# Optimization experiments

Measured on AMD Instinct MI355X. Metric: run time of the kernel, lower is better.

## Reference

```python
import jax, jax.numpy as jnp
import numpy as np

EPS = 1e-5  # torch LayerNorm default


def _ln(x, g, b):
    m = x.mean(-1, keepdims=True)
    v = ((x - m) ** 2).mean(-1, keepdims=True)
    return (x - m) / jnp.sqrt(v + EPS) * g + b


def setup_inputs() -> dict:
    B, T, D, H, L = 4, 2048, 512, 8, 2
    key = jax.random.key(0)
    ks = jax.random.split(key, 16)
    w = lambda k, shp, fan: jax.random.normal(k, shp, jnp.float32) * (fan ** -0.5)
    return {
        "x_vid": jax.random.normal(ks[0], (B, T, D), jnp.float32),
        "x_aud": jax.random.normal(ks[1], (B, T, D), jnp.float32),
        "vid_kpm": jax.random.bernoulli(ks[2], 0.1, (B, T)),
        "aud_kpm": jax.random.bernoulli(ks[3], 0.1, (B, T)),
        "Wq_vid": w(ks[4], (L, D, D), D),
        "Wk_aud_for_vid": w(ks[5], (L, D, D), D),
        "Wq_aud": w(ks[6], (L, D, D), D),
        "Wk_vid_for_aud": w(ks[7], (L, D, D), D),
        "vg_W1": w(ks[8], (L, 2 * H, H), H),
        "vg_b1": jnp.zeros((L, 2 * H), jnp.float32),
        "vg_W2": w(ks[9], (L, 1, 2 * H), 2 * H),
        "vg_b2": jnp.zeros((L, 1), jnp.float32),
        "ag_W1": w(ks[10], (L, 2 * H, H), H),
        "ag_b1": jnp.zeros((L, 2 * H), jnp.float32),
        "ag_W2": w(ks[11], (L, 1, 2 * H), 2 * H),
        "ag_b2": jnp.zeros((L, 1), jnp.float32),
        "vid_ln_g": jnp.ones((L, D), jnp.float32),
        "vid_ln_b": jnp.zeros((L, D), jnp.float32),
        "aud_ln_g": jnp.ones((L, D), jnp.float32),
        "aud_ln_b": jnp.zeros((L, D), jnp.float32),
    }


def reference(x_vid, x_aud, vid_kpm, aud_kpm,
              Wq_vid, Wk_aud_for_vid, Wq_aud, Wk_vid_for_aud,
              vg_W1, vg_b1, vg_W2, vg_b2,
              ag_W1, ag_b1, ag_W2, ag_b2,
              vid_ln_g, vid_ln_b, aud_ln_g, aud_ln_b):
    B, T, D = x_vid.shape
    L = Wq_vid.shape[0]
    H = vg_W1.shape[-1]
    dh = D // H
    scale = dh ** -0.5

    def heads(x):  # (B,T,D) -> (B,H,T,dh)
        return x.reshape(B, T, H, dh).transpose(0, 2, 1, 3)

    # mask-derived constants
    aud_valid = jnp.clip((~aud_kpm).sum(-1).astype(jnp.float32), 1.0)[:, None, None]  # (B,1,1)
    vid_valid = jnp.clip((~vid_kpm).sum(-1).astype(jnp.float32), 1.0)[:, None, None]
    aud_all = aud_kpm.all(-1)  # (B,)
    vid_all = vid_kpm.all(-1)

    def gate_mlp(rel, W1, b1, W2, b2):  # rel: (B,T,H) -> (B,T,1)
        h1 = jax.nn.relu(jnp.einsum('bth,eh->bte', rel, W1) + b1)
        return jax.nn.sigmoid(jnp.einsum('bte,oe->bto', h1, W2) + b2)

    for i in range(L):
        # --- vid gated by attention to aud (NOTE: source applies vid_norms to BOTH) ---
        vid_n = _ln(x_vid, vid_ln_g[i], vid_ln_b[i])
        aud_n = _ln(x_aud, vid_ln_g[i], vid_ln_b[i])
        q = heads(jnp.einsum('btd,od->bto', vid_n, Wq_vid[i]))
        k = heads(jnp.einsum('btd,od->bto', aud_n, Wk_aud_for_vid[i]))
        logits = jnp.einsum('bhtd,bhsd->bhts', q, k) * scale  # (B,H,T,T)
        logits = jnp.where(aud_kpm[:, None, None, :], 0.0, logits)
        rel = logits.sum(-1) / aud_valid           # (B,H,T)
        rel = rel.transpose(0, 2, 1)               # (B,T,H)
        gate_v = gate_mlp(rel, vg_W1[i], vg_b1[i], vg_W2[i], vg_b2[i])
        gate_v = jnp.where(aud_all[:, None, None], 0.0, gate_v)
        x_vid = x_vid + x_vid * gate_v             # dropout is identity at eval

        # --- aud gated by attention to (updated) vid; source applies aud_norms to BOTH ---
        aud_n = _ln(x_aud, aud_ln_g[i], aud_ln_b[i])
        vid_n = _ln(x_vid, aud_ln_g[i], aud_ln_b[i])
        q = heads(jnp.einsum('btd,od->bto', aud_n, Wq_aud[i]))
        k = heads(jnp.einsum('btd,od->bto', vid_n, Wk_vid_for_aud[i]))
        logits = jnp.einsum('bhtd,bhsd->bhts', q, k) * scale
        logits = jnp.where(vid_kpm[:, None, None, :], 0.0, logits)
        rel = (logits.sum(-1) / vid_valid).transpose(0, 2, 1)
        gate_a = gate_mlp(rel, ag_W1[i], ag_b1[i], ag_W2[i], ag_b2[i])
        gate_a = jnp.where(vid_all[:, None, None], 0.0, gate_a)
        x_aud = x_aud + x_aud * gate_a

    return (x_vid, x_aud)
```

## Files before the change

### kernel.cpp

```cpp
#include <hip/hip_runtime.h>
#include <math.h>

#define BB 4
#define TT 2048
#define DD 512
#define HH 8
#define EPS 1e-5f
#define SCALE 0.125f
#define WW ((size_t)DD * DD)


__device__ __forceinline__ float wred(float s) {
#pragma unroll
  for (int o = 32; o > 0; o >>= 1) s += __shfl_xor(s, o);
  return s;
}

__device__ __forceinline__ void ldf(const float* p, int lane, float f[8]) {
  float4 a = *reinterpret_cast<const float4*>(p + lane * 4);
  float4 c = *reinterpret_cast<const float4*>(p + 256 + lane * 4);
  f[0]=a.x; f[1]=a.y; f[2]=a.z; f[3]=a.w;
  f[4]=c.x; f[5]=c.y; f[6]=c.z; f[7]=c.w;
}

__global__ __launch_bounds__(256) void sums_kernel(
    const float* __restrict__ xv, const float* __restrict__ xa,
    const int* __restrict__ vkpm, const int* __restrict__ akpm,
    float* __restrict__ partial)
{
  const int blk  = blockIdx.x;
  const int s    = blk >> 8;
  const int b    = (blk >> 6) & 3;
  const int tile = blk & 63;
  const int wave = threadIdx.x >> 6, lane = threadIdx.x & 63;
  const float* x  = s ? xa : xv;
  const int* kpm  = s ? akpm : vkpm;
  const int row0  = b * TT + tile * 32 + wave * 8;

  __shared__ float lds[4][DD];

  float acc[8] = {0.f,0.f,0.f,0.f,0.f,0.f,0.f,0.f};
  for (int r = 0; r < 8; ++r) {
    const int row = row0 + r;
    float v[8]; ldf(x + (size_t)row * DD, lane, v);
    float s1 = 0.f, s2 = 0.f;
#pragma unroll
    for (int k = 0; k < 8; ++k) { s1 += v[k]; s2 += v[k]*v[k]; }
    s1 = wred(s1); s2 = wred(s2);
    const float mean = s1 * (1.f / (float)DD);
    const float var  = s2 * (1.f / (float)DD) - mean * mean;
    const float rstd = rsqrtf(var + EPS);
    if (kpm[row] == 0) {
#pragma unroll
      for (int k = 0; k < 8; ++k) acc[k] += (v[k] - mean) * rstd;
    }
  }
#pragma unroll
  for (int k = 0; k < 4; ++k) {
    lds[wave][lane*4+k]       = acc[k];
    lds[wave][256+lane*4+k]   = acc[4+k];
  }
  __syncthreads();
  const int tid = threadIdx.x;
  float s0 = lds[0][tid] + lds[1][tid] + lds[2][tid] + lds[3][tid];
  float s1 = lds[0][tid+256] + lds[1][tid+256] + lds[2][tid+256] + lds[3][tid+256];
  float* p = partial + ((size_t)(s*4 + b) * 64 + tile) * DD;
  p[tid]       = s0;
  p[tid + 256] = s1;
}

__global__ __launch_bounds__(256) void reduce_kernel(
    const float* __restrict__ partial,
    const int* __restrict__ vkpm, const int* __restrict__ akpm,
    float* __restrict__ S, float* __restrict__ fs)
{
  const int tid = threadIdx.x, wave = tid >> 6, lane = tid & 63;
  const int job = blockIdx.x * 4 + wave;
  const int sb  = job >> 7;
  const int d0  = (job & 127) * 4;
  __shared__ float csh[4];

  const float* p0 = partial + ((size_t)sb * 64 + lane) * DD + d0;
  float4 a = *reinterpret_cast<const float4*>(p0);
  a.x = wred(a.x); a.y = wred(a.y); a.z = wred(a.z); a.w = wred(a.w);
  if (lane == 0) *reinterpret_cast<float4*>(S + (size_t)sb * DD + d0) = a;

  if (blockIdx.x < 8) {
    const int s = blockIdx.x >> 2, b = blockIdx.x & 3;
    const int* mk = s ? akpm : vkpm;
    int cnt = 0;
#pragma unroll
    for (int q = 0; q < 8; ++q) cnt += (mk[b*TT + q*256 + tid] == 0) ? 1 : 0;
    float fc = wred((float)cnt);
    if (lane == 0) csh[wave] = fc;
    __syncthreads();
    if (tid == 0) {
      const float vc = csh[0] + csh[1] + csh[2] + csh[3];
      fs[blockIdx.x*4 + 0] = SCALE / fmaxf(vc, 1.f);
      fs[blockIdx.x*4 + 1] = (vc > 0.f) ? 1.f : 0.f;
      fs[blockIdx.x*4 + 2] = vc;
    }
  }
}

__global__ __launch_bounds__(256) void mphase_kernel(
    const float* __restrict__ S, const float* __restrict__ fs,
    const float* __restrict__ Wq_v, const float* __restrict__ Wk_av,
    const float* __restrict__ Wq_a, const float* __restrict__ Wk_va,
    const float* __restrict__ vid_g, const float* __restrict__ vid_b,
    const float* __restrict__ aud_g, const float* __restrict__ aud_b,
    float* __restrict__ mp,
    float* __restrict__ cv,
    float* __restrict__ smv)
{
  const int blk = blockIdx.x;
  const int p = blk >> 5, b = (blk >> 3) & 3, h = blk & 7;
  const int layer = p >> 1;
  const int isA = ((p & 1) == 0);
  const int tid = threadIdx.x, wave = tid >> 6, lane = tid & 63;
  __shared__ float ksl[64];
  __shared__ float cs2[4], ss2[4];

  const int ksb = (isA ? 1 : 0) * 4 + b;
  const float* g  = (isA ? vid_g : aud_g) + (size_t)layer * DD;
  const float* be = (isA ? vid_b : aud_b) + (size_t)layer * DD;
  const float* Wk = (isA ? Wk_av : Wk_va) + (size_t)layer * WW;
  const float* Wq = (isA ? Wq_v  : Wq_a ) + (size_t)layer * WW;
  const float fac  = fs[ksb*4 + 0];
  const float cntf = fs[ksb*4 + 2];

  float gv[8], bv[8], sv[8], nl[8];
  ldf(g, lane, gv); ldf(be, lane, bv); ldf(S + (size_t)ksb * DD, lane, sv);
#pragma unroll
  for (int k = 0; k < 8; ++k) nl[k] = sv[k]*gv[k] + cntf*bv[k];

#pragma unroll 4
  for (int jj = 0; jj < 16; ++jj) {
    const int j = wave * 16 + jj;
    float w[8]; ldf(Wk + (size_t)(h*64 + j) * DD, lane, w);
    float sdot = w[0]*nl[0]+w[1]*nl[1]+w[2]*nl[2]+w[3]*nl[3]
               + w[4]*nl[4]+w[5]*nl[5]+w[6]*nl[6]+w[7]*nl[7];
    sdot = wred(sdot);
    if (lane == 0) ksl[j] = sdot * fac;
  }
  __syncthreads();

  float a0 = 0.f, a1 = 0.f;
  const float* base = Wq + (size_t)(h*64) * DD;
#pragma unroll 16
  for (int j = 0; j < 64; ++j) {
    const float kk = ksl[j];
    a0 += base[(size_t)j*DD + tid]       * kk;
    a1 += base[(size_t)j*DD + tid + 256] * kk;
  }

  const float gq0 = g[tid], gq1 = g[tid + 256];
  const float bq0 = be[tid], bq1 = be[tid + 256];
  const float mp0 = a0 * gq0, mp1 = a1 * gq1;
  float* mo = mp + (((size_t)p*4 + b)*8 + h) * DD;
  mo[tid]       = mp0;
  mo[tid + 256] = mp1;

  float cp = a0*bq0 + a1*bq1;
  float sp = mp0 + mp1;
  cp = wred(cp); sp = wred(sp);
  if (lane == 0) { cs2[wave] = cp; ss2[wave] = sp; }
  __syncthreads();
  if (tid == 0) {
    const int idx = ((p*4 + b)*8 + h);
    cv[idx]  = cs2[0]+cs2[1]+cs2[2]+cs2[3];
    smv[idx] = ss2[0]+ss2[1]+ss2[2]+ss2[3];
  }
}

__global__ __launch_bounds__(256) void final_kernel(
    const float* __restrict__ xv_in, const float* __restrict__ xa_in,
    const float* __restrict__ mp, const float* __restrict__ cv,
    const float* __restrict__ smv, const float* __restrict__ fs,
    const float* __restrict__ vg_W1, const float* __restrict__ vg_b1,
    const float* __restrict__ vg_W2, const float* __restrict__ vg_b2,
    const float* __restrict__ ag_W1, const float* __restrict__ ag_b1,
    const float* __restrict__ ag_W2, const float* __restrict__ ag_b2,
    float* __restrict__ out_v, float* __restrict__ out_a)
{
  const int blk = blockIdx.x;
  const int s = blk >> 9, b = (blk >> 7) & 3, tile = blk & 127;
  const int tid = threadIdx.x, lane = tid & 63;
  const int wave = tid >> 6;
  const float* x = s ? xa_in : xv_in;
  float* out     = s ? out_a : out_v;
  const int row0 = b * TT + tile * 16 + wave * 4;

  __shared__ float mlp[2][161];
  {
    const float* W1p = s ? ag_W1 : vg_W1;
    const float* b1p = s ? ag_b1 : vg_b1;
    const float* W2p = s ? ag_W2 : vg_W2;
    const float* b2p = s ? ag_b2 : vg_b2;
    if (tid < 128)       { mlp[0][tid] = W1p[tid];       mlp[1][tid] = W1p[128 + tid]; }
    else if (tid < 144)  { mlp[0][tid] = b1p[tid - 128]; mlp[1][tid] = b1p[tid - 112]; }
    else if (tid < 160)  { mlp[0][tid] = W2p[tid - 144]; mlp[1][tid] = W2p[tid - 128]; }
    else if (tid == 160) { mlp[0][160] = b2p[0];         mlp[1][160] = b2p[1]; }
  }
  __syncthreads();

  const float flag = fs[(((s ? 0 : 1) * 4) + b) * 4 + 1];

  float v[4][8];
  float myMean = 0.f, myRstd = 1.f;
#pragma unroll
  for (int r = 0; r < 4; ++r) {
    ldf(x + (size_t)(row0 + r) * DD, lane, v[r]);
    float s1 = 0.f, s2 = 0.f;
#pragma unroll
    for (int k = 0; k < 8; ++k) { s1 += v[r][k]; s2 += v[r][k]*v[r][k]; }
    s1 = wred(s1); s2 = wred(s2);
    const float mean = s1 * (1.f / (float)DD);
    const float rstd = rsqrtf(s2 * (1.f / (float)DD) - mean*mean + EPS);
    if ((lane & 3) == r) { myMean = mean; myRstd = rstd; }
  }

  float a[64];
  const float* mpb0 = mp + ((size_t)(s*4 + b) * 8) * DD;
  const float* mpb1 = mp + ((size_t)((2+s)*4 + b) * 8) * DD;
#pragma unroll
  for (int l = 0; l < 2; ++l) {
    const float* mb_ = l ? mpb1 : mpb0;
#pragma unroll
    for (int h = 0; h < HH; ++h) {
      float w[8]; ldf(mb_ + (size_t)h * DD, lane, w);
      const int j = l*8 + h;
#pragma unroll
      for (int r = 0; r < 4; ++r) {
        a[r*16 + j] = v[r][0]*w[0] + v[r][1]*w[1] + v[r][2]*w[2] + v[r][3]*w[3]
                    + v[r][4]*w[4] + v[r][5]*w[5] + v[r][6]*w[6] + v[r][7]*w[7];
      }
    }
  }

#pragma unroll
  for (int k = 0; k < 6; ++k) {
    const int bit = (lane >> k) & 1;
#pragma unroll
    for (int m = 0; m < (64 >> (k + 1)); ++m) {
      const float keep = bit ? a[2*m+1] : a[2*m];
      const float send = bit ? a[2*m]   : a[2*m+1];
      a[m] = keep + __shfl_xor(send, 1 << k);
    }
  }

  const int gr = lane & 3, gl = (lane >> 2) & 1;
  float q[8];
#pragma unroll
  for (int h = 0; h < HH; ++h) q[h] = __shfl(a[0], gr*16 + gl*8 + h);

  float gpart = 1.f;
  if (lane < 8) {
    const int l = lane >> 2;
    const int p = l*2 + s;
    const float* cb  = cv  + ((size_t)p*4 + b) * 8;
    const float* sbv = smv + ((size_t)p*4 + b) * 8;
    float rel[8];
#pragma unroll
    for (int h = 0; h < HH; ++h)
      rel[h] = myRstd * (q[h] - myMean * sbv[h]) + cb[h];
    float z = mlp[l][160];
#pragma unroll
    for (int e = 0; e < 16; ++e) {
      float h1 = mlp[l][128 + e];
#pragma unroll
      for (int h = 0; h < HH; ++h) h1 += rel[h] * mlp[l][e*8 + h];
      z += fmaxf(h1, 0.f) * mlp[l][144 + e];
    }
    gpart = 1.f + flag * (1.f / (1.f + expf(-z)));
  }

#pragma unroll
  for (int r = 0; r < 4; ++r) {
    const float sc = __shfl(gpart, r) * __shfl(gpart, 4 + r);
    float* orow = out + (size_t)(row0 + r) * DD;
    *reinterpret_cast<float4*>(orow + lane*4) =
        make_float4(v[r][0]*sc, v[r][1]*sc, v[r][2]*sc, v[r][3]*sc);
    *reinterpret_cast<float4*>(orow + 256 + lane*4) =
        make_float4(v[r][4]*sc, v[r][5]*sc, v[r][6]*sc, v[r][7]*sc);
  }
}

extern "C" void kernel_launch(void* const* d_in, const int* in_sizes, int n_in,
                              void* d_out, int out_size, void* d_ws, size_t ws_size,
                              hipStream_t stream) {
  const float* x_vid = (const float*)d_in[0];
  const float* x_aud = (const float*)d_in[1];
  const int* vid_kpm = (const int*)d_in[2];
  const int* aud_kpm = (const int*)d_in[3];
  const float* Wq_vid         = (const float*)d_in[4];
  const float* Wk_aud_for_vid = (const float*)d_in[5];
  const float* Wq_aud         = (const float*)d_in[6];
  const float* Wk_vid_for_aud = (const float*)d_in[7];
  const float* vg_W1 = (const float*)d_in[8];
  const float* vg_b1 = (const float*)d_in[9];
  const float* vg_W2 = (const float*)d_in[10];
  const float* vg_b2 = (const float*)d_in[11];
  const float* ag_W1 = (const float*)d_in[12];
  const float* ag_b1 = (const float*)d_in[13];
  const float* ag_W2 = (const float*)d_in[14];
  const float* ag_b2 = (const float*)d_in[15];
  const float* vid_ln_g = (const float*)d_in[16];
  const float* vid_ln_b = (const float*)d_in[17];
  const float* aud_ln_g = (const float*)d_in[18];
  const float* aud_ln_b = (const float*)d_in[19];

  const size_t BTD = (size_t)BB * TT * DD;
  float* out_v = (float*)d_out;
  float* out_a = out_v + BTD;

  float* partial = (float*)d_ws;
  float* S       = partial + (size_t)8 * 64 * DD;
  float* fs      = S + (size_t)8 * DD;
  float* mpw     = fs + 32;
  float* cvw     = mpw + (size_t)4 * 4 * 8 * DD;
  float* smw     = cvw + 128;

  sums_kernel<<<512, 256, 0, stream>>>(x_vid, x_aud, vid_kpm, aud_kpm, partial);
  reduce_kernel<<<256, 256, 0, stream>>>(partial, vid_kpm, aud_kpm, S, fs);
  mphase_kernel<<<128, 256, 0, stream>>>(
      S, fs, Wq_vid, Wk_aud_for_vid, Wq_aud, Wk_vid_for_aud,
      vid_ln_g, vid_ln_b, aud_ln_g, aud_ln_b, mpw, cvw, smw);
  final_kernel<<<1024, 256, 0, stream>>>(
      x_vid, x_aud, mpw, cvw, smw, fs,
      vg_W1, vg_b1, vg_W2, vg_b2, ag_W1, ag_b1, ag_W2, ag_b2,
      out_v, out_a);
}
```

Measured before the change: 50.90 us.

## Fuse partial reduction into mphase kernel and halve rows per final block

Removes the separate reduce kernel. Each mphase block now sums the 64 partial tiles for its stream and batch itself, and recounts the mask, saving one launch and the round trip of S through global memory. The cost is redundant work: 16 blocks repeat the same reduction. Separately, final_kernel now handles 2 rows per wave instead of 4 and launches 2048 blocks, which cuts register pressure (a[32] instead of a[64]) and raises parallelism, but loads the MLP weights once per block across twice as many blocks.

```diff
diff --git a/kernel.cpp b/kernel.cpp
--- a/kernel.cpp
+++ b/kernel.cpp
@@ -69,68 +69,83 @@
   p[tid + 256] = s1;
 }
 
-__global__ __launch_bounds__(256) void reduce_kernel(
+__global__ __launch_bounds__(256) void mphase2_kernel(
     const float* __restrict__ partial,
     const int* __restrict__ vkpm, const int* __restrict__ akpm,
-    float* __restrict__ S, float* __restrict__ fs)
-{
-  const int tid = threadIdx.x, wave = tid >> 6, lane = tid & 63;
-  const int job = blockIdx.x * 4 + wave;
-  const int sb  = job >> 7;
-  const int d0  = (job & 127) * 4;
-  __shared__ float csh[4];
-
-  const float* p0 = partial + ((size_t)sb * 64 + lane) * DD + d0;
-  float4 a = *reinterpret_cast<const float4*>(p0);
-  a.x = wred(a.x); a.y = wred(a.y); a.z = wred(a.z); a.w = wred(a.w);
-  if (lane == 0) *reinterpret_cast<float4*>(S + (size_t)sb * DD + d0) = a;
-
-  if (blockIdx.x < 8) {
-    const int s = blockIdx.x >> 2, b = blockIdx.x & 3;
-    const int* mk = s ? akpm : vkpm;
-    int cnt = 0;
-#pragma unroll
-    for (int q = 0; q < 8; ++q) cnt += (mk[b*TT + q*256 + tid] == 0) ? 1 : 0;
-    float fc = wred((float)cnt);
-    if (lane == 0) csh[wave] = fc;
-    __syncthreads();
-    if (tid == 0) {
-      const float vc = csh[0] + csh[1] + csh[2] + csh[3];
-      fs[blockIdx.x*4 + 0] = SCALE / fmaxf(vc, 1.f);
-      fs[blockIdx.x*4 + 1] = (vc > 0.f) ? 1.f : 0.f;
-      fs[blockIdx.x*4 + 2] = vc;
-    }
-  }
-}
-
-__global__ __launch_bounds__(256) void mphase_kernel(
-    const float* __restrict__ S, const float* __restrict__ fs,
     const float* __restrict__ Wq_v, const float* __restrict__ Wk_av,
     const float* __restrict__ Wq_a, const float* __restrict__ Wk_va,
     const float* __restrict__ vid_g, const float* __restrict__ vid_b,
     const float* __restrict__ aud_g, const float* __restrict__ aud_b,
     float* __restrict__ mp,
     float* __restrict__ cv,
-    float* __restrict__ smv)
+    float* __restrict__ smv,
+    float* __restrict__ fs)
 {
   const int blk = blockIdx.x;
   const int p = blk >> 5, b = (blk >> 3) & 3, h = blk & 7;
   const int layer = p >> 1;
   const int isA = ((p & 1) == 0);
   const int tid = threadIdx.x, wave = tid >> 6, lane = tid & 63;
+
+  __shared__ float4 red[256];
+  __shared__ float nsum_s[DD];
   __shared__ float ksl[64];
+  __shared__ float csh[4];
   __shared__ float cs2[4], ss2[4];
 
   const int ksb = (isA ? 1 : 0) * 4 + b;
+
+  {
+    const int half = tid >> 7;
+    const int i    = tid & 127;
+    const float* pp = partial + ((size_t)ksb * 64 + half * 32) * DD + i * 4;
+    float4 acc = make_float4(0.f, 0.f, 0.f, 0.f);
+#pragma unroll 8
+    for (int t = 0; t < 32; ++t) {
+      float4 u = *reinterpret_cast<const float4*>(pp + (size_t)t * DD);
+      acc.x += u.x; acc.y += u.y; acc.z += u.z; acc.w += u.w;
+    }
+    red[tid] = acc;
+  }
+
+  const int* mk = isA ? akpm : vkpm;
+  {
+    int cnt = 0;
+#pragma unroll
+    for (int q = 0; q < 8; ++q) cnt += (mk[b * TT + q * 256 + tid] == 0) ? 1 : 0;
+    float fc = wred((float)cnt);
+    if (lane == 0) csh[wave] = fc;
+  }
+  __syncthreads();
+  if (tid < 128) {
+    float4 a0 = red[tid], a1 = red[tid + 128];
+    *reinterpret_cast<float4*>(&nsum_s[tid * 4]) =
+        make_float4(a0.x + a1.x, a0.y + a1.y, a0.z + a1.z, a0.w + a1.w);
+  }
+  __syncthreads();
+
+  const float vc   = csh[0] + csh[1] + csh[2] + csh[3];
+  const float fac  = SCALE / fmaxf(vc, 1.f);
+  const float cntf = vc;
+  if (layer == 0 && h == 0 && tid == 0) {
+    fs[ksb * 4 + 0] = fac;
+    fs[ksb * 4 + 1] = (vc > 0.f) ? 1.f : 0.f;
+    fs[ksb * 4 + 2] = vc;
+  }
+
   const float* g  = (isA ? vid_g : aud_g) + (size_t)layer * DD;
   const float* be = (isA ? vid_b : aud_b) + (size_t)layer * DD;
   const float* Wk = (isA ? Wk_av : Wk_va) + (size_t)layer * WW;
   const float* Wq = (isA ? Wq_v  : Wq_a ) + (size_t)layer * WW;
-  const float fac  = fs[ksb*4 + 0];
-  const float cntf = fs[ksb*4 + 2];
 
   float gv[8], bv[8], sv[8], nl[8];
-  ldf(g, lane, gv); ldf(be, lane, bv); ldf(S + (size_t)ksb * DD, lane, sv);
+  ldf(g, lane, gv); ldf(be, lane, bv);
+  {
+    float4 a = *reinterpret_cast<const float4*>(&nsum_s[lane * 4]);
+    float4 c = *reinterpret_cast<const float4*>(&nsum_s[256 + lane * 4]);
+    sv[0]=a.x; sv[1]=a.y; sv[2]=a.z; sv[3]=a.w;
+    sv[4]=c.x; sv[5]=c.y; sv[6]=c.z; sv[7]=c.w;
+  }
 #pragma unroll
   for (int k = 0; k < 8; ++k) nl[k] = sv[k]*gv[k] + cntf*bv[k];
 
@@ -184,12 +199,12 @@
     float* __restrict__ out_v, float* __restrict__ out_a)
 {
   const int blk = blockIdx.x;
-  const int s = blk >> 9, b = (blk >> 7) & 3, tile = blk & 127;
+  const int s = blk >> 10, b = (blk >> 8) & 3, tile = blk & 255;
   const int tid = threadIdx.x, lane = tid & 63;
   const int wave = tid >> 6;
   const float* x = s ? xa_in : xv_in;
   float* out     = s ? out_a : out_v;
-  const int row0 = b * TT + tile * 16 + wave * 4;
+  const int row0 = b * TT + tile * 8 + wave * 2;
 
   __shared__ float mlp[2][161];
   {
@@ -206,10 +221,10 @@
 
   const float flag = fs[(((s ? 0 : 1) * 4) + b) * 4 + 1];
 
-  float v[4][8];
+  float v[2][8];
   float myMean = 0.f, myRstd = 1.f;
 #pragma unroll
-  for (int r = 0; r < 4; ++r) {
+  for (int r = 0; r < 2; ++r) {
     ldf(x + (size_t)(row0 + r) * DD, lane, v[r]);
     float s1 = 0.f, s2 = 0.f;
 #pragma unroll
@@ -217,10 +232,10 @@
     s1 = wred(s1); s2 = wred(s2);
     const float mean = s1 * (1.f / (float)DD);
     const float rstd = rsqrtf(s2 * (1.f / (float)DD) - mean*mean + EPS);
-    if ((lane & 3) == r) { myMean = mean; myRstd = rstd; }
-  }
-
-  float a[64];
+    if ((lane & 1) == r) { myMean = mean; myRstd = rstd; }
+  }
+
+  float a[32];
   const float* mpb0 = mp + ((size_t)(s*4 + b) * 8) * DD;
   const float* mpb1 = mp + ((size_t)((2+s)*4 + b) * 8) * DD;
 #pragma unroll
@@ -231,7 +246,7 @@
       float w[8]; ldf(mb_ + (size_t)h * DD, lane, w);
       const int j = l*8 + h;
 #pragma unroll
-      for (int r = 0; r < 4; ++r) {
+      for (int r = 0; r < 2; ++r) {
         a[r*16 + j] = v[r][0]*w[0] + v[r][1]*w[1] + v[r][2]*w[2] + v[r][3]*w[3]
                     + v[r][4]*w[4] + v[r][5]*w[5] + v[r][6]*w[6] + v[r][7]*w[7];
       }
@@ -239,24 +254,25 @@
   }
 
 #pragma unroll
-  for (int k = 0; k < 6; ++k) {
+  for (int k = 0; k < 5; ++k) {
     const int bit = (lane >> k) & 1;
 #pragma unroll
-    for (int m = 0; m < (64 >> (k + 1)); ++m) {
+    for (int m = 0; m < (32 >> (k + 1)); ++m) {
       const float keep = bit ? a[2*m+1] : a[2*m];
       const float send = bit ? a[2*m]   : a[2*m+1];
       a[m] = keep + __shfl_xor(send, 1 << k);
     }
   }
-
-  const int gr = lane & 3, gl = (lane >> 2) & 1;
+  const float dotv = a[0] + __shfl_xor(a[0], 32);
+
+  const int gr = lane & 1, gl = (lane >> 1) & 1;
   float q[8];
 #pragma unroll
-  for (int h = 0; h < HH; ++h) q[h] = __shfl(a[0], gr*16 + gl*8 + h);
+  for (int h = 0; h < HH; ++h) q[h] = __shfl(dotv, gr*16 + gl*8 + h);
 
   float gpart = 1.f;
-  if (lane < 8) {
-    const int l = lane >> 2;
+  if (lane < 4) {
+    const int l = lane >> 1;
     const int p = l*2 + s;
     const float* cb  = cv  + ((size_t)p*4 + b) * 8;
     const float* sbv = smv + ((size_t)p*4 + b) * 8;
@@ -276,8 +292,8 @@
   }
 
 #pragma unroll
-  for (int r = 0; r < 4; ++r) {
-    const float sc = __shfl(gpart, r) * __shfl(gpart, 4 + r);
+  for (int r = 0; r < 2; ++r) {
+    const float sc = __shfl(gpart, r) * __shfl(gpart, 2 + r);
     float* orow = out + (size_t)(row0 + r) * DD;
     *reinterpret_cast<float4*>(orow + lane*4) =
         make_float4(v[r][0]*sc, v[r][1]*sc, v[r][2]*sc, v[r][3]*sc);
@@ -315,18 +331,17 @@
   float* out_a = out_v + BTD;
 
   float* partial = (float*)d_ws;
-  float* S       = partial + (size_t)8 * 64 * DD;
-  float* fs      = S + (size_t)8 * DD;
+  float* fs      = partial + (size_t)8 * 64 * DD;
   float* mpw     = fs + 32;
   float* cvw     = mpw + (size_t)4 * 4 * 8 * DD;
   float* smw     = cvw + 128;
 
   sums_kernel<<<512, 256, 0, stream>>>(x_vid, x_aud, vid_kpm, aud_kpm, partial);
-  reduce_kernel<<<256, 256, 0, stream>>>(partial, vid_kpm, aud_kpm, S, fs);
-  mphase_kernel<<<128, 256, 0, stream>>>(
-      S, fs, Wq_vid, Wk_aud_for_vid, Wq_aud, Wk_vid_for_aud,
-      vid_ln_g, vid_ln_b, aud_ln_g, aud_ln_b, mpw, cvw, smw);
-  final_kernel<<<1024, 256, 0, stream>>>(
+  mphase2_kernel<<<128, 256, 0, stream>>>(
+      partial, vid_kpm, aud_kpm,
+      Wq_vid, Wk_aud_for_vid, Wq_aud, Wk_vid_for_aud,
+      vid_ln_g, vid_ln_b, aud_ln_g, aud_ln_b, mpw, cvw, smw, fs);
+  final_kernel<<<2048, 256, 0, stream>>>(
       x_vid, x_aud, mpw, cvw, smw, fs,
       vg_W1, vg_b1, vg_W2, vg_b2, ag_W1, ag_b1, ag_W2, ag_b2,
       out_v, out_a);
```

Measured after the change: 49.22 us. 1.03x faster.
